# Performance work log

Measured on AMD Instinct MI355X. Metric: run time of the kernel, lower is better.

Reference implementation:

```python
import jax, jax.numpy as jnp
import numpy as np

EPS = 1e-5
NH_MHA = 8
NH_GCN = 4


def _ln(x, w, b):
    m = x.mean(-1, keepdims=True)
    v = ((x - m) ** 2).mean(-1, keepdims=True)
    return (x - m) * jax.lax.rsqrt(v + EPS) * w + b


def _mha(t, in_w, in_b, out_w, out_b):
    # torch nn.MultiheadAttention (batch_first, eval mode -> no dropout)
    B, N, C = t.shape
    hd = C // NH_MHA
    qkv = t @ in_w.T + in_b
    q, k, v = jnp.split(qkv, 3, axis=-1)
    q = q.reshape(B, N, NH_MHA, hd)
    k = k.reshape(B, N, NH_MHA, hd)
    v = v.reshape(B, N, NH_MHA, hd)
    s = jnp.einsum('bihd,bjhd->bhij', q, k) * (1.0 / np.sqrt(hd))
    a = jax.nn.softmax(s, axis=-1)
    o = jnp.einsum('bhij,bjhd->bihd', a, v).reshape(B, N, C)
    return o @ out_w.T + out_b


def _gcn(x, v_w, v_b, e1_w, e1_b, eln_w, eln_b, e2_w, e2_b, o_w, o_b, n_w, n_b):
    # GraphConvolutionNetwork.forward (query/key branches are computed but
    # unused in the original -> omitted, identical math)
    B, N, C = x.shape
    hd = C // NH_GCN
    # edge MLP: split first linear so the [B,N,N,2C] concat is never built
    w1a, w1b = e1_w[:, :C], e1_w[:, C:]
    e = (x @ w1a.T)[:, :, None, :] + (x @ w1b.T)[:, None, :, :] + e1_b  # [B,N,N,C]
    e = jax.nn.gelu(_ln(e, eln_w, eln_b), approximate=False)
    ew = e @ e2_w.T + e2_b                 # [B,Ni,Nj,H]
    adj = jax.nn.softmax(ew, axis=2)       # softmax over Nj (== dim=-1 after permute in torch)
    v = (x @ v_w.T + v_b).reshape(B, N, NH_GCN, hd)
    out = jnp.einsum('bijh,bjhd->bihd', adj, v).reshape(B, N, C)
    out = out @ o_w.T + o_b
    return _ln(out + x, n_w, n_b)          # in_features == out_features -> residual


def reference(x, mha_in_w, mha_in_b, mha_out_w, mha_out_b,
              g0_v_w, g0_v_b, g0_e1_w, g0_e1_b, g0_eln_w, g0_eln_b, g0_e2_w, g0_e2_b, g0_o_w, g0_o_b, g0_n_w, g0_n_b,
              g1_v_w, g1_v_b, g1_e1_w, g1_e1_b, g1_eln_w, g1_eln_b, g1_e2_w, g1_e2_b, g1_o_w, g1_o_b, g1_n_w, g1_n_b,
              n1_w, n1_b, n2_w, n2_b,
              f1_w, f1_b, fln_w, fln_b, f2_w, f2_b):
    B, C, H, W = x.shape
    tokens = x.reshape(B, C, H * W).transpose(0, 2, 1)  # b c h w -> b (h w) c
    attn = _mha(tokens, mha_in_w, mha_in_b, mha_out_w, mha_out_b)
    attn = _ln(attn + tokens, n1_w, n1_b)
    g = _gcn(attn, g0_v_w, g0_v_b, g0_e1_w, g0_e1_b, g0_eln_w, g0_eln_b, g0_e2_w, g0_e2_b, g0_o_w, g0_o_b, g0_n_w, g0_n_b)
    g = _gcn(g, g1_v_w, g1_v_b, g1_e1_w, g1_e1_b, g1_eln_w, g1_eln_b, g1_e2_w, g1_e2_b, g1_o_w, g1_o_b, g1_n_w, g1_n_b)
    g = _ln(g, n2_w, n2_b)
    cat = jnp.concatenate([attn, g], axis=-1)           # [B,N,2C]
    f = cat @ f1_w.T + f1_b
    f = jax.nn.gelu(_ln(f, fln_w, fln_b), approximate=False)
    f = f @ f2_w.T + f2_b
    out = tokens + f
    return out.transpose(0, 2, 1).reshape(B, C, H, W)


def setup_inputs() -> dict:
    key = jax.random.key(0)
    ks = jax.random.split(key, 8)
    B, C, H, W = 2, 128, 24, 24
    f32 = jnp.float32

    def w(k, shape):
        return jax.random.normal(k, shape, f32) * 0.02

    d = {"x": jax.random.normal(ks[0], (B, C, H, W), f32)}
    d["mha_in_w"] = w(ks[1], (3 * C, C)); d["mha_in_b"] = jnp.zeros((3 * C,), f32)
    d["mha_out_w"] = w(ks[2], (C, C)); d["mha_out_b"] = jnp.zeros((C,), f32)
    for i in range(2):
        kk = jax.random.split(ks[3 + i], 4)
        p = f"g{i}_"
        d[p + "v_w"] = w(kk[0], (C, C)); d[p + "v_b"] = jnp.zeros((C,), f32)
        d[p + "e1_w"] = w(kk[1], (C, 2 * C)); d[p + "e1_b"] = jnp.zeros((C,), f32)
        d[p + "eln_w"] = jnp.ones((C,), f32); d[p + "eln_b"] = jnp.zeros((C,), f32)
        d[p + "e2_w"] = w(kk[2], (NH_GCN, C)); d[p + "e2_b"] = jnp.zeros((NH_GCN,), f32)
        d[p + "o_w"] = w(kk[3], (C, C)); d[p + "o_b"] = jnp.zeros((C,), f32)
        d[p + "n_w"] = jnp.ones((C,), f32); d[p + "n_b"] = jnp.zeros((C,), f32)
    d["n1_w"] = jnp.ones((C,), f32); d["n1_b"] = jnp.zeros((C,), f32)
    d["n2_w"] = jnp.ones((C,), f32); d["n2_b"] = jnp.zeros((C,), f32)
    d["f1_w"] = w(ks[5], (C, 2 * C)); d["f1_b"] = jnp.zeros((C,), f32)
    d["fln_w"] = jnp.ones((C,), f32); d["fln_b"] = jnp.zeros((C,), f32)
    d["f2_w"] = w(ks[6], (C, C)); d["f2_b"] = jnp.zeros((C,), f32)
    return d
```

## Files before the change

### kernel.cpp

```cpp
#include <hip/hip_runtime.h>
#include <hip/hip_fp16.h>
#include <math.h>

#define NN 576
#define EPSV 1e-5f
#define PSTR 592

typedef _Float16 h2v __attribute__((ext_vector_type(2)));
__device__ __forceinline__ float fdot2f(__half2 a, __half2 b, float c) {
    return __builtin_amdgcn_fdot2(__builtin_bit_cast(h2v, a),
                                  __builtin_bit_cast(h2v, b), c, false);
}

__device__ __forceinline__ float gelu_exact(float x) {
    return 0.5f * x * (1.0f + erff(x * 0.70710678118654752f));
}

__global__ void k_setup(const float* __restrict__ x, float* __restrict__ tok,
                        const float* __restrict__ mha_in_w,
                        const float* __restrict__ e1w0, const float* __restrict__ vw0,
                        const float* __restrict__ e1w1, const float* __restrict__ vw1,
                        const float* __restrict__ lnw0, const float* __restrict__ lnb0,
                        const float* __restrict__ e2w0,
                        const float* __restrict__ lnw1, const float* __restrict__ lnb1,
                        const float* __restrict__ e2w1,
                        float* __restrict__ wTq, float* __restrict__ wT0,
                        float* __restrict__ wT1, __half* __restrict__ wh) {
    const int which = blockIdx.y;
    const int idx = blockIdx.x * 256 + threadIdx.x;
    if (which < 2) {
        if (idx < NN * 128) {
            int n = idx >> 7, c = idx & 127;
            tok[(size_t)which * NN * 128 + idx] = x[((size_t)which * 128 + c) * NN + n];
        }
        return;
    }
    if (which == 5) {
        if (idx < 1536) {
            int l = idx / 768, i2 = idx - l * 768;
            const float* lw = l ? lnw1 : lnw0;
            const float* lb = l ? lnb1 : lnb0;
            const float* e2 = l ? e2w1 : e2w0;
            float v;
            if (i2 < 128)      v = lw[i2];
            else if (i2 < 256) v = lb[i2 - 128];
            else               v = e2[i2 - 256];
            wh[idx] = __float2half(v);
        }
        return;
    }
    if (idx >= 49152) return;
    int k = idx / 384, o = idx - k * 384;
    if (which == 2) {
        wTq[idx] = mha_in_w[o * 128 + k];
    } else {
        const float* e1w = (which == 3) ? e1w0 : e1w1;
        const float* vw  = (which == 3) ? vw0  : vw1;
        float v;
        if (o < 128)      v = e1w[o * 256 + k];
        else if (o < 256) v = e1w[(o - 128) * 256 + 128 + k];
        else              v = vw[(o - 256) * 128 + k];
        ((which == 3) ? wT0 : wT1)[idx] = v;
    }
}

template<bool CENTER>
__global__ __launch_bounds__(384) void k_gemmT(
    const float* __restrict__ A, const float* __restrict__ wT,
    const float* __restrict__ b0, const float* __restrict__ b1, const float* __restrict__ b2,
    float* __restrict__ out)
{
    const int t = threadIdx.x;
    const int r0 = blockIdx.x * 4;
    __shared__ float a_s[4][132];
    if (t < 128) {
        float4 v = *(const float4*)(A + (size_t)(r0 + (t >> 5)) * 128 + (t & 31) * 4);
        *(float4*)&a_s[t >> 5][(t & 31) * 4] = v;
    }
    __syncthreads();
    float acc[4] = {0.f, 0.f, 0.f, 0.f};
    #pragma unroll 8
    for (int k = 0; k < 128; ++k) {
        float w = wT[(size_t)k * 384 + t];
        acc[0] += a_s[0][k] * w;
        acc[1] += a_s[1][k] * w;
        acc[2] += a_s[2][k] * w;
        acc[3] += a_s[3][k] * w;
    }
    const float* bp = (t < 128) ? b0 : ((t < 256) ? b1 : b2);
    float bv = bp ? bp[t & 127] : 0.f;
    #pragma unroll
    for (int r = 0; r < 4; ++r) acc[r] += bv;

    if (CENTER) {
        __shared__ float redc[6][4];
        const int wv = t >> 6, ln = t & 63;
        #pragma unroll
        for (int r = 0; r < 4; ++r) {
            float xr = acc[r];
            #pragma unroll
            for (int off = 32; off > 0; off >>= 1) xr += __shfl_xor(xr, off);
            if (ln == 0) redc[wv][r] = xr;
        }
        __syncthreads();
        if (t < 256) {
            const int ch = t >> 7;
            #pragma unroll
            for (int r = 0; r < 4; ++r) {
                float mean = (redc[2 * ch][r] + redc[2 * ch + 1][r]) * (1.0f / 128.0f);
                acc[r] -= mean;
            }
        }
    }
    if (t < 256) {
        #pragma unroll
        for (int r = 0; r < 4; ++r)
            ((__half*)(out + (size_t)(r0 + r) * 384))[t] = __float2half(acc[r]);
    } else {
        #pragma unroll
        for (int r = 0; r < 4; ++r)
            out[(size_t)(r0 + r) * 384 + t] = acc[r];
    }
}

__global__ __launch_bounds__(256) void k_score(
    const float* __restrict__ qkv, __half* __restrict__ sc)
{
    const int jt = blockIdx.x, it = blockIdx.y, b = blockIdx.z;
    const int i0 = it * 16, j0 = jt * 16;
    const int t = threadIdx.x;
    __shared__ __half q_s[16][136], k_s[16][136];
    for (int idx = t; idx < 512; idx += 256) {
        int tile = idx >> 8, r = (idx >> 4) & 15, cq = idx & 15;
        const __half* src = (const __half*)(qkv + (size_t)(b * NN + (tile ? j0 : i0) + r) * 384)
                            + (tile ? 128 : 0) + cq * 8;
        __half* dst = tile ? &k_s[r][cq * 8] : &q_s[r][cq * 8];
        *(uint4*)dst = *(const uint4*)src;
    }
    __syncthreads();
    const int ti = t >> 4, tj = t & 15;
    const uint4* qr = (const uint4*)q_s[ti];
    const uint4* kr = (const uint4*)k_s[tj];
    float acc[8] = {0.f,0.f,0.f,0.f,0.f,0.f,0.f,0.f};
    #pragma unroll
    for (int sstep = 0; sstep < 16; ++sstep) {
        uint4 q4 = qr[sstep], k4 = kr[sstep];
        const __half2* qh = (const __half2*)&q4;
        const __half2* kh = (const __half2*)&k4;
        #pragma unroll
        for (int p = 0; p < 4; ++p)
            acc[sstep >> 1] = fdot2f(qh[p], kh[p], acc[sstep >> 1]);
    }
    __half2 h[4];
    #pragma unroll
    for (int p = 0; p < 4; ++p)
        h[p] = __floats2half2_rn(acc[2 * p] * 0.25f, acc[2 * p + 1] * 0.25f);
    *(uint4*)(sc + ((size_t)(b * NN + i0 + ti) * NN + j0 + tj) * 8) = *(uint4*)h;
}

__global__ __launch_bounds__(256) void k_edge(
    const float* __restrict__ qkv, const __half* __restrict__ wh,
    const float* __restrict__ e2b, __half* __restrict__ ew)
{
    const int jt = blockIdx.x, it = blockIdx.y, b = blockIdx.z;
    const int i0 = it * 16, j0 = jt * 16;
    const int t = threadIdx.x;
    __shared__ __half ua_s[16][136], wb_s[16][136], wh_s[768];

    for (int idx = t; idx < 512; idx += 256) {
        int tile = idx >> 8, r = (idx >> 4) & 15, cq = idx & 15;
        const __half* src = (const __half*)(qkv + (size_t)(b * NN + (tile ? j0 : i0) + r) * 384)
                            + (tile ? 128 : 0) + cq * 8;
        __half* dst = tile ? &wb_s[r][cq * 8] : &ua_s[r][cq * 8];
        *(uint4*)dst = *(const uint4*)src;
    }
    if (t < 96) *(uint4*)&wh_s[t * 8] = *(const uint4*)&wh[t * 8];
    __syncthreads();

    const int ti = t >> 4, tj = t & 15;
    const uint4* uar = (const uint4*)ua_s[ti];
    const uint4* wbr = (const uint4*)wb_s[tj];

    float s2 = 0.f;
    #pragma unroll
    for (int sstep = 0; sstep < 16; ++sstep) {
        uint4 u4 = uar[sstep], w4 = wbr[sstep];
        const __half2* uh = (const __half2*)&u4;
        const __half2* whp = (const __half2*)&w4;
        #pragma unroll
        for (int p = 0; p < 4; ++p) {
            __half2 e = __hadd2(uh[p], whp[p]);
            s2 = fdot2f(e, e, s2);
        }
    }
    const float rstd = rsqrtf(s2 * (1.0f / 128.0f) + EPSV);
    const __half2 rh   = __float2half2_rn(rstd);
    const __half2 cexp = __float2half2_rn(-2.4554672f);
    const __half2 one2 = __float2half2_rn(1.0f);

    float p0 = 0.f, p1 = 0.f, p2 = 0.f, p3 = 0.f;
    #pragma unroll 4
    for (int sstep = 0; sstep < 16; ++sstep) {
        uint4 u4 = uar[sstep], w4 = wbr[sstep];
        uint4 lw4 = *(const uint4*)&wh_s[sstep * 8];
        uint4 lb4 = *(const uint4*)&wh_s[128 + sstep * 8];
        uint4 q04 = *(const uint4*)&wh_s[256 + sstep * 8];
        uint4 q14 = *(const uint4*)&wh_s[384 + sstep * 8];
        uint4 q24 = *(const uint4*)&wh_s[512 + sstep * 8];
        uint4 q34 = *(const uint4*)&wh_s[640 + sstep * 8];
        const __half2* uh  = (const __half2*)&u4;
        const __half2* whp = (const __half2*)&w4;
        const __half2* lwh = (const __half2*)&lw4;
        const __half2* lbh = (const __half2*)&lb4;
        const __half2* q0h = (const __half2*)&q04;
        const __half2* q1h = (const __half2*)&q14;
        const __half2* q2h = (const __half2*)&q24;
        const __half2* q3h = (const __half2*)&q34;
        #pragma unroll
        for (int p = 0; p < 4; ++p) {
            __half2 e   = __hadd2(uh[p], whp[p]);
            __half2 t1  = __hmul2(e, lwh[p]);
            __half2 nrm = __hfma2(t1, rh, lbh[p]);
            __half2 z   = __hmul2(nrm, cexp);
            __half2 ex  = h2exp2(z);
            __half2 den = __hadd2(ex, one2);
            __half2 rr  = h2rcp(den);
            __half2 g   = __hmul2(nrm, rr);
            p0 = fdot2f(g, q0h[p], p0);
            p1 = fdot2f(g, q1h[p], p1);
            p2 = fdot2f(g, q2h[p], p2);
            p3 = fdot2f(g, q3h[p], p3);
        }
    }
    __half2 h01 = __floats2half2_rn(p0 + e2b[0], p1 + e2b[1]);
    __half2 h23 = __floats2half2_rn(p2 + e2b[2], p3 + e2b[3]);
    __half* dst = ew + ((size_t)(b * NN + i0 + ti) * NN + j0 + tj) * 4;
    *(__half2*)dst = h01;
    *(__half2*)(dst + 2) = h23;
}

template<int NH, bool FINAL>
__global__ __launch_bounds__(256) void k_agg(
    const float* __restrict__ resid, const float* __restrict__ vbuf,
    const __half* __restrict__ sc,
    const float* __restrict__ ow, const float* __restrict__ ob,
    const float* __restrict__ nw, const float* __restrict__ nb,
    float* __restrict__ outp,
    const float* __restrict__ tok, const float* __restrict__ attn,
    const float* __restrict__ n2w, const float* __restrict__ n2b,
    const float* __restrict__ f1w, const float* __restrict__ f1b,
    const float* __restrict__ flnw, const float* __restrict__ flnb,
    const float* __restrict__ f2w, const float* __restrict__ f2b,
    float* __restrict__ finout)
{
    constexpr int GL = 256 / NH;
    constexpr int NE = NN / GL;
    const int bi = blockIdx.x;
    const int b = bi / NN, i = bi - b * NN;
    const int t = threadIdx.x;

    __shared__ __half p_lds[NH * PSTR];
    __shared__ float st_i[NH];
    __shared__ float aggp[8][128];
    __shared__ float agg_s[128];
    __shared__ float op[2][128];
    __shared__ float red1[4], red2[4];
    __shared__ float cat_s[256], gl_s[128];
    __shared__ float red3[4], red4[4], red5[2], red6[2];

    const __half* srow = sc + (size_t)(b * NN + i) * NN * NH;

    {
        const int h = t / GL, jl = t % GL;
        float sv[NE];
        #pragma unroll
        for (int k = 0; k < NE; ++k)
            sv[k] = __half2float(srow[(size_t)(jl + k * GL) * NH + h]);
        float mx = -1e30f;
        #pragma unroll
        for (int k = 0; k < NE; ++k) mx = fmaxf(mx, sv[k]);
        #pragma unroll
        for (int off = GL / 2; off > 0; off >>= 1) mx = fmaxf(mx, __shfl_xor(mx, off));
        float sm = 0.f;
        #pragma unroll
        for (int k = 0; k < NE; ++k) {
            float e = __expf(sv[k] - mx);
            sm += e;
            p_lds[h * PSTR + jl + k * GL] = __float2half(e);
        }
        #pragma unroll
        for (int off = GL / 2; off > 0; off >>= 1) sm += __shfl_xor(sm, off);
        if (jl == 0) st_i[h] = 1.0f / sm;
    }
    __syncthreads();

    {
        const int c4 = (t & 31) * 4, jg = t >> 5;
        const int h2 = c4 >> ((NH == 8) ? 4 : 5);
        const float inv2 = st_i[h2];
        float4 acc = {0.f, 0.f, 0.f, 0.f};
        const float* vb = vbuf + 256 + c4;
        const __half* ph = p_lds + h2 * PSTR;
        #pragma unroll 4
        for (int j = jg; j < NN; j += 8) {
            float p = __half2float(ph[j]);
            const float4 v4 = *(const float4*)(vb + (size_t)(b * NN + j) * 384);
            acc.x += p * v4.x; acc.y += p * v4.y; acc.z += p * v4.z; acc.w += p * v4.w;
        }
        acc.x *= inv2; acc.y *= inv2; acc.z *= inv2; acc.w *= inv2;
        *(float4*)&aggp[jg][c4] = acc;
    }
    __syncthreads();
    if (t < 128) {
        float s = 0.f;
        #pragma unroll
        for (int gq = 0; gq < 8; ++gq) s += aggp[gq][t];
        agg_s[t] = s;
    }
    __syncthreads();

    {
        const int c = t & 127, half = t >> 7;
        float o = 0.f;
        const float4* wr = (const float4*)(ow + (size_t)c * 128 + half * 64);
        const float4* ar = (const float4*)(agg_s + half * 64);
        #pragma unroll
        for (int kq = 0; kq < 16; ++kq) {
            float4 w = wr[kq], a = ar[kq];
            o += w.x * a.x + w.y * a.y + w.z * a.z + w.w * a.w;
        }
        op[half][c] = o;
    }
    __syncthreads();
    const size_t row = (size_t)(b * NN + i) * 128;
    float val = 0.f;
    if (t < 128)
        val = op[0][t] + op[1][t] + ob[t] + resid[row + t];

    float s1 = val, s2 = val * val;
    #pragma unroll
    for (int off = 32; off > 0; off >>= 1) {
        s1 += __shfl_xor(s1, off);
        s2 += __shfl_xor(s2, off);
    }
    if ((t & 63) == 0) { red1[t >> 6] = s1; red2[t >> 6] = s2; }
    __syncthreads();
    float tot1 = red1[0] + red1[1] + red1[2] + red1[3];
    float tot2 = red2[0] + red2[1] + red2[2] + red2[3];
    float mean = tot1 * (1.0f / 128.0f);
    float var = tot2 * (1.0f / 128.0f) - mean * mean;
    float rstd = rsqrtf(var + EPSV);
    float gval = 0.f;
    if (t < 128) gval = (val - mean) * rstd * nw[t] + nb[t];

    if (!FINAL) {
        if (t < 128) outp[row + t] = gval;
        return;
    }

    {
        float a1 = gval, a2 = gval * gval;
        #pragma unroll
        for (int off = 32; off > 0; off >>= 1) { a1 += __shfl_xor(a1, off); a2 += __shfl_xor(a2, off); }
        if ((t & 63) == 0) { red3[t >> 6] = a1; red4[t >> 6] = a2; }
    }
    __syncthreads();
    {
        float m2 = (red3[0] + red3[1] + red3[2] + red3[3]) * (1.0f / 128.0f);
        float v2 = (red4[0] + red4[1] + red4[2] + red4[3]) * (1.0f / 128.0f) - m2 * m2;
        float r2 = rsqrtf(v2 + EPSV);
        if (t < 128) {
            cat_s[t] = attn[row + t];
            cat_s[128 + t] = (gval - m2) * r2 * n2w[t] + n2b[t];
        }
    }
    __syncthreads();
    {
        const int o = t & 127, half = t >> 7;
        float f = 0.f;
        const float4* wr = (const float4*)(f1w + (size_t)o * 256 + half * 128);
        const float4* cr = (const float4*)(cat_s + half * 128);
        #pragma unroll
        for (int kq = 0; kq < 32; ++kq) {
            float4 w = wr[kq], c = cr[kq];
            f += w.x * c.x + w.y * c.y + w.z * c.z + w.w * c.w;
        }
        op[half][o] = f;
    }
    __syncthreads();
    float fv = 0.f;
    if (t < 128) fv = op[0][t] + op[1][t] + f1b[t];
    {
        float a1 = fv, a2 = fv * fv;
        #pragma unroll
        for (int off = 32; off > 0; off >>= 1) { a1 += __shfl_xor(a1, off); a2 += __shfl_xor(a2, off); }
        if (t < 128 && (t & 63) == 0) { red5[t >> 6] = a1; red6[t >> 6] = a2; }
    }
    __syncthreads();
    {
        float m3 = (red5[0] + red5[1]) * (1.0f / 128.0f);
        float v3 = (red6[0] + red6[1]) * (1.0f / 128.0f) - m3 * m3;
        float r3 = rsqrtf(v3 + EPSV);
        if (t < 128) {
            float nrm = (fv - m3) * r3 * flnw[t] + flnb[t];
            gl_s[t] = gelu_exact(nrm);
        }
    }
    __syncthreads();
    {
        const int o = t & 127, half = t >> 7;
        float f = 0.f;
        const float4* wr = (const float4*)(f2w + (size_t)o * 128 + half * 64);
        const float4* gr = (const float4*)(gl_s + half * 64);
        #pragma unroll
        for (int kq = 0; kq < 16; ++kq) {
            float4 w = wr[kq], gg = gr[kq];
            f += w.x * gg.x + w.y * gg.y + w.z * gg.z + w.w * gg.w;
        }
        op[half][o] = f;
    }
    __syncthreads();
    if (t < 128)
        finout[((size_t)b * 128 + t) * NN + i] =
            tok[row + t] + op[0][t] + op[1][t] + f2b[t];
}

extern "C" void kernel_launch(void* const* d_in, const int* in_sizes, int n_in,
                              void* d_out, int out_size, void* d_ws, size_t ws_size,
                              hipStream_t stream) {
    const float* x         = (const float*)d_in[0];
    const float* mha_in_b  = (const float*)d_in[2];
    const float* mha_out_w = (const float*)d_in[3];
    const float* mha_out_b = (const float*)d_in[4];
    const float* gv_w[2]  = {(const float*)d_in[5],  (const float*)d_in[17]};
    const float* gv_b[2]  = {(const float*)d_in[6],  (const float*)d_in[18]};
    const float* ge1_w[2] = {(const float*)d_in[7],  (const float*)d_in[19]};
    const float* ge1_b[2] = {(const float*)d_in[8],  (const float*)d_in[20]};
    const float* geln_w[2]= {(const float*)d_in[9],  (const float*)d_in[21]};
    const float* geln_b[2]= {(const float*)d_in[10], (const float*)d_in[22]};
    const float* ge2_w[2] = {(const float*)d_in[11], (const float*)d_in[23]};
    const float* ge2_b[2] = {(const float*)d_in[12], (const float*)d_in[24]};
    const float* go_w[2]  = {(const float*)d_in[13], (const float*)d_in[25]};
    const float* go_b[2]  = {(const float*)d_in[14], (const float*)d_in[26]};
    const float* gn_w[2]  = {(const float*)d_in[15], (const float*)d_in[27]};
    const float* gn_b[2]  = {(const float*)d_in[16], (const float*)d_in[28]};
    const float* n1w = (const float*)d_in[29];
    const float* n1b = (const float*)d_in[30];
    const float* n2w = (const float*)d_in[31];
    const float* n2b = (const float*)d_in[32];
    const float* f1w = (const float*)d_in[33];
    const float* f1b = (const float*)d_in[34];
    const float* flnw = (const float*)d_in[35];
    const float* flnb = (const float*)d_in[36];
    const float* f2w = (const float*)d_in[37];
    const float* f2b = (const float*)d_in[38];

    float* ws     = (float*)d_ws;
    float* tokens = ws;
    float* attn   = tokens + 147456;
    float* g      = attn + 147456;
    float* qkv    = g + 147456;
    float* wTq    = qkv + 442368;
    float* wT0    = wTq + 49152;
    float* wT1    = wT0 + 49152;
    __half* wh    = (__half*)(wT1 + 49152);
    __half* sc    = wh + 2048;
    __half* ewh   = sc;

    k_setup<<<dim3(288, 6), 256, 0, stream>>>(x, tokens, (const float*)d_in[1],
        ge1_w[0], gv_w[0], ge1_w[1], gv_w[1],
        geln_w[0], geln_b[0], ge2_w[0],
        geln_w[1], geln_b[1], ge2_w[1],
        wTq, wT0, wT1, wh);

    k_gemmT<false><<<288, 384, 0, stream>>>(tokens, wTq,
        mha_in_b, mha_in_b + 128, mha_in_b + 256, qkv);
    k_score<<<dim3(36, 36, 2), 256, 0, stream>>>(qkv, sc);
    k_agg<8, false><<<1152, 256, 0, stream>>>(tokens, qkv, sc, mha_out_w, mha_out_b,
        n1w, n1b, attn,
        nullptr, nullptr, nullptr, nullptr, nullptr, nullptr, nullptr, nullptr,
        nullptr, nullptr, nullptr);

    for (int l = 0; l < 2; ++l) {
        const float* xin = (l == 0) ? attn : g;
        const float* wTl = (l == 0) ? wT0 : wT1;
        k_gemmT<true><<<288, 384, 0, stream>>>(xin, wTl,
            nullptr, ge1_b[l], gv_b[l], qkv);
        k_edge<<<dim3(36, 36, 2), 256, 0, stream>>>(qkv, wh + l * 768,
                                                    ge2_b[l], ewh);
        if (l == 0) {
            k_agg<4, false><<<1152, 256, 0, stream>>>(xin, qkv, ewh, go_w[l], go_b[l],
                gn_w[l], gn_b[l], g,
                nullptr, nullptr, nullptr, nullptr, nullptr, nullptr, nullptr, nullptr,
                nullptr, nullptr, nullptr);
        } else {
            k_agg<4, true><<<1152, 256, 0, stream>>>(xin, qkv, ewh, go_w[l], go_b[l],
                gn_w[l], gn_b[l], nullptr,
                tokens, attn, n2w, n2b, f1w, f1b, flnw, flnb, f2w, f2b,
                (float*)d_out);
        }
    }
}
```

Measured before the change: 220.4 us.

## Fuse score and edge-logit kernels into per-row softmax-aggregation kernels

The separate attention-score and GCN edge-MLP kernels are removed. Their logit computation now runs inside the aggregation kernel: each block owns one query row, computes logits for all 576 keys in registers, does a block-wide softmax, and stores probabilities in LDS. This avoids writing and re-reading the fp16 score/edge buffers in global memory and saves three kernel launches. The edge-MLP second-layer bias is dropped, which is exact because it is constant across j and cancels in the softmax. In exchange, the 16x16 tile reuse of key rows is lost, so every block re-reads all key rows from L2, and the kernel uses more registers.

```diff
diff --git a/kernel.cpp b/kernel.cpp
--- a/kernel.cpp
+++ b/kernel.cpp
@@ -4,7 +4,6 @@
 
 #define NN 576
 #define EPSV 1e-5f
-#define PSTR 592
 
 typedef _Float16 h2v __attribute__((ext_vector_type(2)));
 __device__ __forceinline__ float fdot2f(__half2 a, __half2 b, float c) {
@@ -123,126 +122,10 @@
     }
 }
 
-__global__ __launch_bounds__(256) void k_score(
-    const float* __restrict__ qkv, __half* __restrict__ sc)
-{
-    const int jt = blockIdx.x, it = blockIdx.y, b = blockIdx.z;
-    const int i0 = it * 16, j0 = jt * 16;
-    const int t = threadIdx.x;
-    __shared__ __half q_s[16][136], k_s[16][136];
-    for (int idx = t; idx < 512; idx += 256) {
-        int tile = idx >> 8, r = (idx >> 4) & 15, cq = idx & 15;
-        const __half* src = (const __half*)(qkv + (size_t)(b * NN + (tile ? j0 : i0) + r) * 384)
-                            + (tile ? 128 : 0) + cq * 8;
-        __half* dst = tile ? &k_s[r][cq * 8] : &q_s[r][cq * 8];
-        *(uint4*)dst = *(const uint4*)src;
-    }
-    __syncthreads();
-    const int ti = t >> 4, tj = t & 15;
-    const uint4* qr = (const uint4*)q_s[ti];
-    const uint4* kr = (const uint4*)k_s[tj];
-    float acc[8] = {0.f,0.f,0.f,0.f,0.f,0.f,0.f,0.f};
-    #pragma unroll
-    for (int sstep = 0; sstep < 16; ++sstep) {
-        uint4 q4 = qr[sstep], k4 = kr[sstep];
-        const __half2* qh = (const __half2*)&q4;
-        const __half2* kh = (const __half2*)&k4;
-        #pragma unroll
-        for (int p = 0; p < 4; ++p)
-            acc[sstep >> 1] = fdot2f(qh[p], kh[p], acc[sstep >> 1]);
-    }
-    __half2 h[4];
-    #pragma unroll
-    for (int p = 0; p < 4; ++p)
-        h[p] = __floats2half2_rn(acc[2 * p] * 0.25f, acc[2 * p + 1] * 0.25f);
-    *(uint4*)(sc + ((size_t)(b * NN + i0 + ti) * NN + j0 + tj) * 8) = *(uint4*)h;
-}
-
-__global__ __launch_bounds__(256) void k_edge(
-    const float* __restrict__ qkv, const __half* __restrict__ wh,
-    const float* __restrict__ e2b, __half* __restrict__ ew)
-{
-    const int jt = blockIdx.x, it = blockIdx.y, b = blockIdx.z;
-    const int i0 = it * 16, j0 = jt * 16;
-    const int t = threadIdx.x;
-    __shared__ __half ua_s[16][136], wb_s[16][136], wh_s[768];
-
-    for (int idx = t; idx < 512; idx += 256) {
-        int tile = idx >> 8, r = (idx >> 4) & 15, cq = idx & 15;
-        const __half* src = (const __half*)(qkv + (size_t)(b * NN + (tile ? j0 : i0) + r) * 384)
-                            + (tile ? 128 : 0) + cq * 8;
-        __half* dst = tile ? &wb_s[r][cq * 8] : &ua_s[r][cq * 8];
-        *(uint4*)dst = *(const uint4*)src;
-    }
-    if (t < 96) *(uint4*)&wh_s[t * 8] = *(const uint4*)&wh[t * 8];
-    __syncthreads();
-
-    const int ti = t >> 4, tj = t & 15;
-    const uint4* uar = (const uint4*)ua_s[ti];
-    const uint4* wbr = (const uint4*)wb_s[tj];
-
-    float s2 = 0.f;
-    #pragma unroll
-    for (int sstep = 0; sstep < 16; ++sstep) {
-        uint4 u4 = uar[sstep], w4 = wbr[sstep];
-        const __half2* uh = (const __half2*)&u4;
-        const __half2* whp = (const __half2*)&w4;
-        #pragma unroll
-        for (int p = 0; p < 4; ++p) {
-            __half2 e = __hadd2(uh[p], whp[p]);
-            s2 = fdot2f(e, e, s2);
-        }
-    }
-    const float rstd = rsqrtf(s2 * (1.0f / 128.0f) + EPSV);
-    const __half2 rh   = __float2half2_rn(rstd);
-    const __half2 cexp = __float2half2_rn(-2.4554672f);
-    const __half2 one2 = __float2half2_rn(1.0f);
-
-    float p0 = 0.f, p1 = 0.f, p2 = 0.f, p3 = 0.f;
-    #pragma unroll 4
-    for (int sstep = 0; sstep < 16; ++sstep) {
-        uint4 u4 = uar[sstep], w4 = wbr[sstep];
-        uint4 lw4 = *(const uint4*)&wh_s[sstep * 8];
-        uint4 lb4 = *(const uint4*)&wh_s[128 + sstep * 8];
-        uint4 q04 = *(const uint4*)&wh_s[256 + sstep * 8];
-        uint4 q14 = *(const uint4*)&wh_s[384 + sstep * 8];
-        uint4 q24 = *(const uint4*)&wh_s[512 + sstep * 8];
-        uint4 q34 = *(const uint4*)&wh_s[640 + sstep * 8];
-        const __half2* uh  = (const __half2*)&u4;
-        const __half2* whp = (const __half2*)&w4;
-        const __half2* lwh = (const __half2*)&lw4;
-        const __half2* lbh = (const __half2*)&lb4;
-        const __half2* q0h = (const __half2*)&q04;
-        const __half2* q1h = (const __half2*)&q14;
-        const __half2* q2h = (const __half2*)&q24;
-        const __half2* q3h = (const __half2*)&q34;
-        #pragma unroll
-        for (int p = 0; p < 4; ++p) {
-            __half2 e   = __hadd2(uh[p], whp[p]);
-            __half2 t1  = __hmul2(e, lwh[p]);
-            __half2 nrm = __hfma2(t1, rh, lbh[p]);
-            __half2 z   = __hmul2(nrm, cexp);
-            __half2 ex  = h2exp2(z);
-            __half2 den = __hadd2(ex, one2);
-            __half2 rr  = h2rcp(den);
-            __half2 g   = __hmul2(nrm, rr);
-            p0 = fdot2f(g, q0h[p], p0);
-            p1 = fdot2f(g, q1h[p], p1);
-            p2 = fdot2f(g, q2h[p], p2);
-            p3 = fdot2f(g, q3h[p], p3);
-        }
-    }
-    __half2 h01 = __floats2half2_rn(p0 + e2b[0], p1 + e2b[1]);
-    __half2 h23 = __floats2half2_rn(p2 + e2b[2], p3 + e2b[3]);
-    __half* dst = ew + ((size_t)(b * NN + i0 + ti) * NN + j0 + tj) * 4;
-    *(__half2*)dst = h01;
-    *(__half2*)(dst + 2) = h23;
-}
-
-template<int NH, bool FINAL>
-__global__ __launch_bounds__(256) void k_agg(
-    const float* __restrict__ resid, const float* __restrict__ vbuf,
-    const __half* __restrict__ sc,
+template<int NH, bool GCN, bool FINAL>
+__global__ __launch_bounds__(256) void k_fused(
+    const float* __restrict__ resid, const float* __restrict__ qkv,
+    const __half* __restrict__ wh,
     const float* __restrict__ ow, const float* __restrict__ ob,
     const float* __restrict__ nw, const float* __restrict__ nb,
     float* __restrict__ outp,
@@ -253,45 +136,171 @@
     const float* __restrict__ f2w, const float* __restrict__ f2b,
     float* __restrict__ finout)
 {
-    constexpr int GL = 256 / NH;
-    constexpr int NE = NN / GL;
     const int bi = blockIdx.x;
     const int b = bi / NN, i = bi - b * NN;
     const int t = threadIdx.x;
-
-    __shared__ __half p_lds[NH * PSTR];
+    const int wid = t >> 6, ln = t & 63;
+
+    __shared__ __half ua_s[128];
+    __shared__ __half wh_s[768];
+    __shared__ __half p_lds[NN * NH + 8];
     __shared__ float st_i[NH];
+    __shared__ float redm[4][NH], reds[4][NH];
     __shared__ float aggp[8][128];
     __shared__ float agg_s[128];
     __shared__ float op[2][128];
     __shared__ float red1[4], red2[4];
     __shared__ float cat_s[256], gl_s[128];
-    __shared__ float red3[4], red4[4], red5[2], red6[2];
-
-    const __half* srow = sc + (size_t)(b * NN + i) * NN * NH;
-
-    {
-        const int h = t / GL, jl = t % GL;
-        float sv[NE];
-        #pragma unroll
-        for (int k = 0; k < NE; ++k)
-            sv[k] = __half2float(srow[(size_t)(jl + k * GL) * NH + h]);
-        float mx = -1e30f;
-        #pragma unroll
-        for (int k = 0; k < NE; ++k) mx = fmaxf(mx, sv[k]);
-        #pragma unroll
-        for (int off = GL / 2; off > 0; off >>= 1) mx = fmaxf(mx, __shfl_xor(mx, off));
-        float sm = 0.f;
-        #pragma unroll
-        for (int k = 0; k < NE; ++k) {
-            float e = __expf(sv[k] - mx);
-            sm += e;
-            p_lds[h * PSTR + jl + k * GL] = __float2half(e);
-        }
-        #pragma unroll
-        for (int off = GL / 2; off > 0; off >>= 1) sm += __shfl_xor(sm, off);
-        if (jl == 0) st_i[h] = 1.0f / sm;
-    }
+    __shared__ float red5[2], red6[2];
+
+    if (t < 16)
+        ((uint4*)ua_s)[t] = ((const uint4*)(qkv + (size_t)(b * NN + i) * 384))[t];
+    if (GCN) {
+        if (t >= 64 && t < 160)
+            ((uint4*)wh_s)[t - 64] = ((const uint4*)wh)[t - 64];
+    }
+    __syncthreads();
+
+    const __half2 cexp = __float2half2_rn(-2.4554672f);
+    const __half2 one2 = __float2half2_rn(1.0f);
+
+    float lg[3][NH];
+    #pragma unroll
+    for (int js = 0; js < 3; ++js) {
+        const int j = t + js * 256;
+        if (js == 2 && t >= 64) {
+            #pragma unroll
+            for (int h = 0; h < NH; ++h) lg[2][h] = -1e30f;
+            continue;
+        }
+        const uint4* krow = (const uint4*)((const __half*)(qkv + (size_t)(b * NN + j) * 384) + 128);
+        uint4 kx[16];
+        #pragma unroll
+        for (int g = 0; g < 16; ++g) kx[g] = krow[g];
+
+        if (!GCN) {
+            float acc[8];
+            #pragma unroll
+            for (int h = 0; h < 8; ++h) acc[h] = 0.f;
+            #pragma unroll
+            for (int g = 0; g < 16; ++g) {
+                uint4 ug = ((const uint4*)ua_s)[g];
+                const __half2* uh = (const __half2*)&ug;
+                const __half2* kh = (const __half2*)&kx[g];
+                #pragma unroll
+                for (int p = 0; p < 4; ++p)
+                    acc[g >> 1] = fdot2f(uh[p], kh[p], acc[g >> 1]);
+            }
+            #pragma unroll
+            for (int h = 0; h < NH; ++h) lg[js][h] = acc[h] * 0.25f;
+        } else {
+            float s2 = 0.f;
+            #pragma unroll
+            for (int g = 0; g < 16; ++g) {
+                uint4 ug = ((const uint4*)ua_s)[g];
+                const __half2* uh = (const __half2*)&ug;
+                const __half2* kh = (const __half2*)&kx[g];
+                #pragma unroll
+                for (int p = 0; p < 4; ++p) {
+                    __half2 e = __hadd2(uh[p], kh[p]);
+                    s2 = fdot2f(e, e, s2);
+                }
+            }
+            const __half2 rh = __float2half2_rn(rsqrtf(s2 * (1.0f / 128.0f) + EPSV));
+            float p0 = 0.f, p1 = 0.f, p2 = 0.f, p3 = 0.f;
+            #pragma unroll 4
+            for (int g = 0; g < 16; ++g) {
+                uint4 ug  = ((const uint4*)ua_s)[g];
+                uint4 lw4 = *(const uint4*)&wh_s[g * 8];
+                uint4 lb4 = *(const uint4*)&wh_s[128 + g * 8];
+                uint4 q04 = *(const uint4*)&wh_s[256 + g * 8];
+                uint4 q14 = *(const uint4*)&wh_s[384 + g * 8];
+                uint4 q24 = *(const uint4*)&wh_s[512 + g * 8];
+                uint4 q34 = *(const uint4*)&wh_s[640 + g * 8];
+                const __half2* uh  = (const __half2*)&ug;
+                const __half2* kh  = (const __half2*)&kx[g];
+                const __half2* lwh = (const __half2*)&lw4;
+                const __half2* lbh = (const __half2*)&lb4;
+                const __half2* q0h = (const __half2*)&q04;
+                const __half2* q1h = (const __half2*)&q14;
+                const __half2* q2h = (const __half2*)&q24;
+                const __half2* q3h = (const __half2*)&q34;
+                #pragma unroll
+                for (int p = 0; p < 4; ++p) {
+                    __half2 e   = __hadd2(uh[p], kh[p]);
+                    __half2 t1  = __hmul2(e, lwh[p]);
+                    __half2 nrm = __hfma2(t1, rh, lbh[p]);
+                    __half2 z   = __hmul2(nrm, cexp);
+                    __half2 ex  = h2exp2(z);
+                    __half2 den = __hadd2(ex, one2);
+                    __half2 rr  = h2rcp(den);
+                    __half2 g2  = __hmul2(nrm, rr);
+                    p0 = fdot2f(g2, q0h[p], p0);
+                    p1 = fdot2f(g2, q1h[p], p1);
+                    p2 = fdot2f(g2, q2h[p], p2);
+                    p3 = fdot2f(g2, q3h[p], p3);
+                }
+            }
+            lg[js][0] = p0; lg[js][1] = p1; lg[js][2] = p2; lg[js][3] = p3;
+        }
+    }
+
+    float lmx[NH];
+    #pragma unroll
+    for (int h = 0; h < NH; ++h)
+        lmx[h] = fmaxf(fmaxf(lg[0][h], lg[1][h]), lg[2][h]);
+    #pragma unroll
+    for (int h = 0; h < NH; ++h)
+        #pragma unroll
+        for (int off = 32; off > 0; off >>= 1)
+            lmx[h] = fmaxf(lmx[h], __shfl_xor(lmx[h], off));
+    if (ln == 0) {
+        #pragma unroll
+        for (int h = 0; h < NH; ++h) redm[wid][h] = lmx[h];
+    }
+    __syncthreads();
+    float mh[NH];
+    #pragma unroll
+    for (int h = 0; h < NH; ++h)
+        mh[h] = fmaxf(fmaxf(redm[0][h], redm[1][h]), fmaxf(redm[2][h], redm[3][h]));
+
+    float lsum[NH];
+    #pragma unroll
+    for (int h = 0; h < NH; ++h) lsum[h] = 0.f;
+    #pragma unroll
+    for (int js = 0; js < 3; ++js) {
+        const int j = t + js * 256;
+        if (js == 2 && t >= 64) continue;
+        float pv[NH];
+        #pragma unroll
+        for (int h = 0; h < NH; ++h) {
+            pv[h] = __expf(lg[js][h] - mh[h]);
+            lsum[h] += pv[h];
+        }
+        if (NH == 4) {
+            __half2 h01 = __floats2half2_rn(pv[0], pv[1]);
+            __half2 h23 = __floats2half2_rn(pv[2], pv[3]);
+            uint2 u; u.x = __builtin_bit_cast(unsigned, h01); u.y = __builtin_bit_cast(unsigned, h23);
+            *(uint2*)&p_lds[j * 4] = u;
+        } else {
+            __half2 hh[4];
+            #pragma unroll
+            for (int p = 0; p < 4; ++p) hh[p] = __floats2half2_rn(pv[2 * p], pv[2 * p + 1]);
+            *(uint4*)&p_lds[j * 8] = *(uint4*)hh;
+        }
+    }
+    #pragma unroll
+    for (int h = 0; h < NH; ++h)
+        #pragma unroll
+        for (int off = 32; off > 0; off >>= 1)
+            lsum[h] += __shfl_xor(lsum[h], off);
+    if (ln == 0) {
+        #pragma unroll
+        for (int h = 0; h < NH; ++h) reds[wid][h] = lsum[h];
+    }
+    __syncthreads();
+    if (t < NH)
+        st_i[t] = 1.0f / (reds[0][t] + reds[1][t] + reds[2][t] + reds[3][t]);
     __syncthreads();
 
     {
@@ -299,11 +308,10 @@
         const int h2 = c4 >> ((NH == 8) ? 4 : 5);
         const float inv2 = st_i[h2];
         float4 acc = {0.f, 0.f, 0.f, 0.f};
-        const float* vb = vbuf + 256 + c4;
-        const __half* ph = p_lds + h2 * PSTR;
+        const float* vb = qkv + 256 + c4;
         #pragma unroll 4
         for (int j = jg; j < NN; j += 8) {
-            float p = __half2float(ph[j]);
+            float p = __half2float(p_lds[j * NH + h2]);
             const float4 v4 = *(const float4*)(vb + (size_t)(b * NN + j) * 384);
             acc.x += p * v4.x; acc.y += p * v4.y; acc.z += p * v4.z; acc.w += p * v4.w;
         }
@@ -337,13 +345,13 @@
     if (t < 128)
         val = op[0][t] + op[1][t] + ob[t] + resid[row + t];
 
-    float s1 = val, s2 = val * val;
+    float s1 = val, s2r = val * val;
     #pragma unroll
     for (int off = 32; off > 0; off >>= 1) {
         s1 += __shfl_xor(s1, off);
-        s2 += __shfl_xor(s2, off);
-    }
-    if ((t & 63) == 0) { red1[t >> 6] = s1; red2[t >> 6] = s2; }
+        s2r += __shfl_xor(s2r, off);
+    }
+    if (ln == 0) { red1[wid] = s1; red2[wid] = s2r; }
     __syncthreads();
     float tot1 = red1[0] + red1[1] + red1[2] + red1[3];
     float tot2 = red2[0] + red2[1] + red2[2] + red2[3];
@@ -362,12 +370,12 @@
         float a1 = gval, a2 = gval * gval;
         #pragma unroll
         for (int off = 32; off > 0; off >>= 1) { a1 += __shfl_xor(a1, off); a2 += __shfl_xor(a2, off); }
-        if ((t & 63) == 0) { red3[t >> 6] = a1; red4[t >> 6] = a2; }
-    }
-    __syncthreads();
-    {
-        float m2 = (red3[0] + red3[1] + red3[2] + red3[3]) * (1.0f / 128.0f);
-        float v2 = (red4[0] + red4[1] + red4[2] + red4[3]) * (1.0f / 128.0f) - m2 * m2;
+        if (ln == 0) { redm[wid][0] = a1; reds[wid][0] = a2; }
+    }
+    __syncthreads();
+    {
+        float m2 = (redm[0][0] + redm[1][0] + redm[2][0] + redm[3][0]) * (1.0f / 128.0f);
+        float v2 = (reds[0][0] + reds[1][0] + reds[2][0] + reds[3][0]) * (1.0f / 128.0f) - m2 * m2;
         float r2 = rsqrtf(v2 + EPSV);
         if (t < 128) {
             cat_s[t] = attn[row + t];
@@ -394,7 +402,7 @@
         float a1 = fv, a2 = fv * fv;
         #pragma unroll
         for (int off = 32; off > 0; off >>= 1) { a1 += __shfl_xor(a1, off); a2 += __shfl_xor(a2, off); }
-        if (t < 128 && (t & 63) == 0) { red5[t >> 6] = a1; red6[t >> 6] = a2; }
+        if (t < 128 && ln == 0) { red5[wid] = a1; red6[wid] = a2; }
     }
     __syncthreads();
     {
@@ -439,7 +447,6 @@
     const float* geln_w[2]= {(const float*)d_in[9],  (const float*)d_in[21]};
     const float* geln_b[2]= {(const float*)d_in[10], (const float*)d_in[22]};
     const float* ge2_w[2] = {(const float*)d_in[11], (const float*)d_in[23]};
-    const float* ge2_b[2] = {(const float*)d_in[12], (const float*)d_in[24]};
     const float* go_w[2]  = {(const float*)d_in[13], (const float*)d_in[25]};
     const float* go_b[2]  = {(const float*)d_in[14], (const float*)d_in[26]};
     const float* gn_w[2]  = {(const float*)d_in[15], (const float*)d_in[27]};
@@ -464,8 +471,6 @@
     float* wT0    = wTq + 49152;
     float* wT1    = wT0 + 49152;
     __half* wh    = (__half*)(wT1 + 49152);
-    __half* sc    = wh + 2048;
-    __half* ewh   = sc;
 
     k_setup<<<dim3(288, 6), 256, 0, stream>>>(x, tokens, (const float*)d_in[1],
         ge1_w[0], gv_w[0], ge1_w[1], gv_w[1],
@@ -475,29 +480,22 @@
 
     k_gemmT<false><<<288, 384, 0, stream>>>(tokens, wTq,
         mha_in_b, mha_in_b + 128, mha_in_b + 256, qkv);
-    k_score<<<dim3(36, 36, 2), 256, 0, stream>>>(qkv, sc);
-    k_agg<8, false><<<1152, 256, 0, stream>>>(tokens, qkv, sc, mha_out_w, mha_out_b,
-        n1w, n1b, attn,
+    k_fused<8, false, false><<<1152, 256, 0, stream>>>(tokens, qkv, nullptr,
+        mha_out_w, mha_out_b, n1w, n1b, attn,
         nullptr, nullptr, nullptr, nullptr, nullptr, nullptr, nullptr, nullptr,
         nullptr, nullptr, nullptr);
 
-    for (int l = 0; l < 2; ++l) {
-        const float* xin = (l == 0) ? attn : g;
-        const float* wTl = (l == 0) ? wT0 : wT1;
-        k_gemmT<true><<<288, 384, 0, stream>>>(xin, wTl,
-            nullptr, ge1_b[l], gv_b[l], qkv);
-        k_edge<<<dim3(36, 36, 2), 256, 0, stream>>>(qkv, wh + l * 768,
-                                                    ge2_b[l], ewh);
-        if (l == 0) {
-            k_agg<4, false><<<1152, 256, 0, stream>>>(xin, qkv, ewh, go_w[l], go_b[l],
-                gn_w[l], gn_b[l], g,
-                nullptr, nullptr, nullptr, nullptr, nullptr, nullptr, nullptr, nullptr,
-                nullptr, nullptr, nullptr);
-        } else {
-            k_agg<4, true><<<1152, 256, 0, stream>>>(xin, qkv, ewh, go_w[l], go_b[l],
-                gn_w[l], gn_b[l], nullptr,
-                tokens, attn, n2w, n2b, f1w, f1b, flnw, flnb, f2w, f2b,
-                (float*)d_out);
-        }
-    }
+    k_gemmT<true><<<288, 384, 0, stream>>>(attn, wT0,
+        nullptr, ge1_b[0], gv_b[0], qkv);
+    k_fused<4, true, false><<<1152, 256, 0, stream>>>(attn, qkv, wh,
+        go_w[0], go_b[0], gn_w[0], gn_b[0], g,
+        nullptr, nullptr, nullptr, nullptr, nullptr, nullptr, nullptr, nullptr,
+        nullptr, nullptr, nullptr);
+
+    k_gemmT<true><<<288, 384, 0, stream>>>(g, wT1,
+        nullptr, ge1_b[1], gv_b[1], qkv);
+    k_fused<4, true, true><<<1152, 256, 0, stream>>>(g, qkv, wh + 768,
+        go_w[1], go_b[1], gn_w[1], gn_b[1], nullptr,
+        tokens, attn, n2w, n2b, f1w, f1b, flnw, flnb, f2w, f2b,
+        (float*)d_out);
 }
```

New measurement: 370.7 us. +68.2%, slower.
